# Performance work log

Hardware: AMD Instinct MI355X
Metric: run time of the kernel (lower is better)

## Reference

```python
import jax, jax.numpy as jnp
import numpy as np

VOL = 100.0  # cubic volume (100,100,100)


def _forward(x, positions, input_weights, features, output_weights,
             connection_radii, thresholds, n_iterations):
    # clamp positions into the volume (per-axis, min 0.1, max VOL-0.1)
    pos = jnp.clip(positions, 0.1, VOL - 0.1)                      # [N,3]
    radii = jnp.clip(connection_radii, 1.0, 50.0)                  # [N]
    # pairwise Euclidean distances via ||a||^2 + ||b||^2 - 2ab (avoids [N,N,3])
    sq = jnp.sum(pos * pos, axis=1)
    d2 = jnp.maximum(sq[:, None] + sq[None, :] - 2.0 * (pos @ pos.T), 0.0)
    pos_mask = d2 > 0.0
    dist = jnp.where(pos_mask, jnp.sqrt(jnp.where(pos_mask, d2, 1.0)), 0.0)  # [N,N]
    max_r = jnp.max(radii)
    conn_mask = (dist < max_r).astype(dist.dtype)
    atten = jnp.exp(-jnp.minimum(dist / (radii[:, None] + 1e-6), 20.0)) * conn_mask
    # feature similarity (F.normalize uses eps as a clamp-min on the norm)
    fn = features / jnp.maximum(jnp.linalg.norm(features, axis=1, keepdims=True), 1e-6)
    feat_sim = fn @ fn.T                                            # [N,N]
    cw = atten * (0.3 + 0.7 * jnp.clip(feat_sim, -1.0, 1.0))
    cw = cw / (jnp.sum(cw, axis=1, keepdims=True) + 1e-6)           # row-normalized [N,N]
    # spatial input / output gating along x-axis
    xc = jnp.clip(pos[:, 0] / VOL, 0.0, 1.0)                        # [N]
    iw = jnp.exp(-3.0 * xc)
    iw = iw / (jnp.sum(iw) + 1e-6)
    act = (x @ input_weights.T) * iw                                # [B,N]
    for _ in range(n_iterations):
        act = jnp.minimum(jax.nn.relu(act + act @ cw.T - thresholds), 100.0)
    ow = jnp.exp(3.0 * (xc - 1.0))
    ow = ow / (jnp.sum(ow) + 1e-6)
    return (act * ow) @ output_weights                              # [B,out]


def setup_inputs() -> dict:
    key = jax.random.key(0)
    ks = jax.random.split(key, 5)
    N, IN, OUT, FD, B = 8000, 784, 10, 32, 64
    return {
        "x": jax.random.normal(ks[0], (B, IN), jnp.float32),
        "positions": jax.random.uniform(ks[1], (N, 3), jnp.float32) * VOL,
        "input_weights": jax.random.normal(ks[2], (N, IN), jnp.float32) * 0.01,
        "features": jax.random.normal(ks[3], (N, FD), jnp.float32) * 0.1,
        "output_weights": jax.random.normal(ks[4], (N, OUT), jnp.float32) * 0.01,
        "connection_radii": jnp.ones((N,), jnp.float32) * 15.0,
        "thresholds": jnp.zeros((N,), jnp.float32),
        "n_iterations": 2,
    }


def reference(x, positions, input_weights, features, output_weights,
              connection_radii, thresholds, n_iterations):
    return _forward(x, positions, input_weights, features, output_weights,
                    connection_radii, thresholds, n_iterations)
```

## Files before the change

### kernel.cpp

```cpp
#include <hip/hip_runtime.h>
#include <hip/hip_bf16.h>
#include <math.h>

#define VOLF 100.0f
#define FD 32
#define OUT_DIM 10
#define MAXN 320
#define MAX_LAUNCH_ITERS 4
#define KSPLIT 7
#define ITILE 8
#define OB 128

__global__ __launch_bounds__(256) void k_pre(
    const float* __restrict__ positions, const float* __restrict__ radii_in,
    const float* __restrict__ features, float* __restrict__ posx4,
    float* __restrict__ radii, float* __restrict__ e_iw, float* __restrict__ e_ow,
    float* __restrict__ fn, float* __restrict__ scal, int N)
{
    int i = blockIdx.x * blockDim.x + threadIdx.x;
    float my_iw = 0.0f, my_ow = 0.0f, my_r = 0.0f;
    if (i < N) {
        float px = fminf(fmaxf(positions[3*i+0], 0.1f), VOLF - 0.1f);
        float py = fminf(fmaxf(positions[3*i+1], 0.1f), VOLF - 0.1f);
        float pz = fminf(fmaxf(positions[3*i+2], 0.1f), VOLF - 0.1f);
        float sq = px*px + py*py + pz*pz;
        posx4[4*i+0] = px; posx4[4*i+1] = py; posx4[4*i+2] = pz; posx4[4*i+3] = sq;
        float r = fminf(fmaxf(radii_in[i], 1.0f), 50.0f);
        radii[i] = r; my_r = r;
        float xc = fminf(fmaxf(px / VOLF, 0.0f), 1.0f);
        my_iw = expf(-3.0f * xc);
        my_ow = expf(3.0f * (xc - 1.0f));
        e_iw[i] = my_iw; e_ow[i] = my_ow;
        float s = 0.0f;
        #pragma unroll
        for (int k = 0; k < FD; k++) { float v = features[(size_t)i*FD + k]; s += v*v; }
        float nrm = fmaxf(sqrtf(s), 1e-6f);
        #pragma unroll
        for (int k = 0; k < FD; k++) fn[(size_t)i*FD + k] = features[(size_t)i*FD + k] / nrm;
    }
    __shared__ float red[256];
    red[threadIdx.x] = my_iw; __syncthreads();
    for (int s = 128; s > 0; s >>= 1) { if (threadIdx.x < s) red[threadIdx.x] += red[threadIdx.x + s]; __syncthreads(); }
    if (threadIdx.x == 0) atomicAdd(&scal[0], red[0]);
    __syncthreads();
    red[threadIdx.x] = my_ow; __syncthreads();
    for (int s = 128; s > 0; s >>= 1) { if (threadIdx.x < s) red[threadIdx.x] += red[threadIdx.x + s]; __syncthreads(); }
    if (threadIdx.x == 0) atomicAdd(&scal[1], red[0]);
    if (i < N) atomicMax((int*)&scal[2], __float_as_int(my_r));
}

__global__ __launch_bounds__(256) void k_xt(const float* __restrict__ x, float* __restrict__ xT,
                                            int B, int IN)
{
    int idx = blockIdx.x * blockDim.x + threadIdx.x;
    if (idx < B * IN) {
        int b = idx / IN, k = idx % IN;
        xT[(size_t)k * B + b] = x[idx];
    }
}

__global__ __launch_bounds__(256) void k_act0(
    const float* __restrict__ xT, const float* __restrict__ Wi,
    float* __restrict__ partial, int N, int IN)
{
    int wave = threadIdx.x >> 6, lane = threadIdx.x & 63;
    int i0 = blockIdx.x * 32 + wave * 8;
    int kchunk = IN / KSPLIT;
    int k0 = blockIdx.y * kchunk;
    int k1 = k0 + kchunk;
    float acc[8] = {0,0,0,0,0,0,0,0};
    for (int k = k0; k < k1; k += 4) {
        float xv0 = xT[(size_t)(k+0) * 64 + lane];
        float xv1 = xT[(size_t)(k+1) * 64 + lane];
        float xv2 = xT[(size_t)(k+2) * 64 + lane];
        float xv3 = xT[(size_t)(k+3) * 64 + lane];
        #pragma unroll
        for (int n = 0; n < 8; n++) {
            const float4 w = *(const float4*)(Wi + (size_t)(i0 + n) * IN + k);
            acc[n] += w.x * xv0 + w.y * xv1 + w.z * xv2 + w.w * xv3;
        }
    }
    #pragma unroll
    for (int n = 0; n < 8; n++)
        partial[((size_t)blockIdx.y * N + (i0 + n)) * 64 + lane] = acc[n];
}

__global__ __launch_bounds__(256) void k_act0_red(
    const float* __restrict__ partial, const float* __restrict__ e_iw,
    const float* __restrict__ scal, float* __restrict__ actA, int N)
{
    int idx = blockIdx.x * 256 + threadIdx.x;
    int i = idx >> 6;
    size_t stride = (size_t)N * 64;
    float s = 0.0f;
    #pragma unroll
    for (int ks = 0; ks < KSPLIT; ks++) s += partial[ks * stride + idx];
    float inv = 1.0f / (scal[0] + 1e-6f);
    actA[idx] = s * (e_iw[i] * inv);
}

__global__ __launch_bounds__(256) void k_scan(
    const float* __restrict__ posx4, const float* __restrict__ scal,
    int* __restrict__ nbr_idx, float* __restrict__ nbr_w ,
    int* __restrict__ nbr_cnt, int N)
{
    int i0 = blockIdx.x * ITILE;
    __shared__ int cnt[ITILE];
    if (threadIdx.x < ITILE) cnt[threadIdx.x] = 0;
    __syncthreads();
    float4 pi[ITILE];
    #pragma unroll
    for (int t = 0; t < ITILE; t++) pi[t] = ((const float4*)posx4)[i0 + t];
    float maxr = __int_as_float(((const int*)scal)[2]);
    for (int j = threadIdx.x; j < N; j += 256) {
        float4 pj = ((const float4*)posx4)[j];
        #pragma unroll
        for (int t = 0; t < ITILE; t++) {
            float d2 = fmaxf(pi[t].w + pj.w - 2.0f*(pi[t].x*pj.x + pi[t].y*pj.y + pi[t].z*pj.z), 0.0f);
            float dist = (d2 > 0.0f) ? sqrtf(d2) : 0.0f;
            if (dist < maxr) {
                int pos = atomicAdd(&cnt[t], 1);
                if (pos < MAXN) {
                    nbr_idx[(size_t)(i0+t) * MAXN + pos] = j;
                    nbr_w [(size_t)(i0+t) * MAXN + pos] = dist;
                }
            }
        }
    }
    __syncthreads();
    if (threadIdx.x < ITILE) nbr_cnt[i0 + threadIdx.x] = min(cnt[threadIdx.x], MAXN);
}

__global__ __launch_bounds__(128) void k_weight(
    const float* __restrict__ fn, const float* __restrict__ radii,
    const int* __restrict__ nbr_idx, float* __restrict__ nbr_w ,
    const int* __restrict__ nbr_cnt, float* __restrict__ rowinv, int N)
{
    int i = blockIdx.x;
    __shared__ float4 fni[FD/4];
    __shared__ float red[128];
    if (threadIdx.x < FD/4) fni[threadIdx.x] = ((const float4*)(fn + (size_t)i * FD))[threadIdx.x];
    __syncthreads();
    float inv_ri = 1.0f / (radii[i] + 1e-6f);
    int cnt = nbr_cnt[i];
    float s = 0.0f;
    for (int e = threadIdx.x; e < cnt; e += 128) {
        int j     = nbr_idx[(size_t)i * MAXN + e];
        float dist= nbr_w [(size_t)i * MAXN + e];
        const float4* fnj = (const float4*)(fn + (size_t)j * FD);
        float fs = 0.0f;
        #pragma unroll
        for (int k = 0; k < FD/4; k++) {
            float4 a = fni[k], b = fnj[k];
            fs += a.x*b.x + a.y*b.y + a.z*b.z + a.w*b.w;
        }
        fs = fminf(fmaxf(fs, -1.0f), 1.0f);
        float w = expf(-fminf(dist * inv_ri, 20.0f)) * (0.3f + 0.7f * fs);
        nbr_w[(size_t)i * MAXN + e] = w;
        s += w;
    }
    red[threadIdx.x] = s; __syncthreads();
    for (int st = 64; st > 0; st >>= 1) { if (threadIdx.x < st) red[threadIdx.x] += red[threadIdx.x + st]; __syncthreads(); }
    if (threadIdx.x == 0) rowinv[i] = 1.0f / (red[0] + 1e-6f);
}

__global__ __launch_bounds__(256) void k_iter(
    const float* __restrict__ actIn, float* __restrict__ actOut,
    const int* __restrict__ nbr_idx, const float* __restrict__ nbr_w,
    const int* __restrict__ nbr_cnt, const float* __restrict__ rowinv,
    const float* __restrict__ thr,
    const int* __restrict__ nIterPtr, int iterIdx, int N)
{
    if (iterIdx >= min(*nIterPtr, MAX_LAUNCH_ITERS)) return;
    int i = blockIdx.x;
    int wave = threadIdx.x >> 6, lane = threadIdx.x & 63;
    int cnt = nbr_cnt[i];
    float acc = 0.0f;
    for (int e = wave; e < cnt; e += 4) {
        int j   = nbr_idx[(size_t)i * MAXN + e];
        float w = nbr_w [(size_t)i * MAXN + e];
        acc += actIn[(size_t)j * 64 + lane] * w;
    }
    __shared__ float redA[4 * 64];
    redA[wave * 64 + lane] = acc;
    __syncthreads();
    if (wave == 0) {
        float tot = redA[lane] + redA[64 + lane] + redA[128 + lane] + redA[192 + lane];
        float v = actIn[(size_t)i * 64 + lane] + tot * rowinv[i] - thr[i];
        v = fminf(fmaxf(v, 0.0f), 100.0f);
        actOut[(size_t)i * 64 + lane] = v;
    }
}

__global__ __launch_bounds__(256) void k_out1(
    const float* __restrict__ actA, const float* __restrict__ actB,
    const int* __restrict__ nIterPtr, const float* __restrict__ e_ow,
    const float* __restrict__ scal, const float* __restrict__ outW,
    float* __restrict__ outPart, int N)
{
    int m = min(*nIterPtr, MAX_LAUNCH_ITERS);
    const float* actF = (m & 1) ? actB : actA;
    int wave = threadIdx.x >> 6, lane = threadIdx.x & 63;
    float inv = 1.0f / (scal[1] + 1e-6f);
    float acc[OUT_DIM];
    #pragma unroll
    for (int o = 0; o < OUT_DIM; o++) acc[o] = 0.0f;
    for (int i = blockIdx.x * 4 + wave; i < N; i += OB * 4) {
        float a = actF[(size_t)i * 64 + lane] * (e_ow[i] * inv);
        const float* wo = outW + (size_t)i * OUT_DIM;
        #pragma unroll
        for (int o = 0; o < OUT_DIM; o++) acc[o] += a * wo[o];
    }
    __shared__ float red[4][OUT_DIM][64];
    #pragma unroll
    for (int o = 0; o < OUT_DIM; o++) red[wave][o][lane] = acc[o];
    __syncthreads();
    if (wave == 0) {
        #pragma unroll
        for (int o = 0; o < OUT_DIM; o++) {
            float s = red[0][o][lane] + red[1][o][lane] + red[2][o][lane] + red[3][o][lane];
            outPart[((size_t)blockIdx.x * OUT_DIM + o) * 64 + lane] = s;
        }
    }
}

__global__ __launch_bounds__(256) void k_out2(
    const float* __restrict__ outPart, float* __restrict__ out)
{
    int t = blockIdx.x * 256 + threadIdx.x;
    if (t >= 64 * OUT_DIM) return;
    int b = t / OUT_DIM, o = t % OUT_DIM;
    float s = 0.0f;
    for (int blk = 0; blk < OB; blk++)
        s += outPart[((size_t)blk * OUT_DIM + o) * 64 + b];
    out[t] = s;
}

extern "C" void kernel_launch(void* const* d_in, const int* in_sizes, int n_in,
                              void* d_out, int out_size, void* d_ws, size_t ws_size,
                              hipStream_t stream)
{
    const float* x        = (const float*)d_in[0];
    const float* positions= (const float*)d_in[1];
    const float* Win      = (const float*)d_in[2];
    const float* features = (const float*)d_in[3];
    const float* Wout     = (const float*)d_in[4];
    const float* radii_in = (const float*)d_in[5];
    const float* thr      = (const float*)d_in[6];
    const int*   nIter    = (const int*)  d_in[7];

    const int N  = in_sizes[5];
    const int IN = in_sizes[2] / N;
    const int B  = in_sizes[0] / IN;
    (void)B;

    float* ws = (float*)d_ws;
    size_t off = 0;
    auto alloc = [&](size_t nfloats) { size_t cur = off; off += (nfloats + 63) & ~(size_t)63; return cur; };
    float* xT      = ws + alloc((size_t)B * IN);
    float* posx4   = ws + alloc((size_t)N * 4);
    float* radii   = ws + alloc(N);
    float* e_iw    = ws + alloc(N);
    float* e_ow    = ws + alloc(N);
    float* rowinv  = ws + alloc(N);
    float* scal    = ws + alloc(4);
    float* outPart = ws + alloc((size_t)OB * OUT_DIM * 64);
    float* fn      = ws + alloc((size_t)N * FD);
    float* actA    = ws + alloc((size_t)N * 64);
    float* actB    = ws + alloc((size_t)N * 64);
    float* nbr_w   = ws + alloc((size_t)N * MAXN);
    int*   nbr_idx = (int*)(ws + alloc((size_t)N * MAXN));
    int*   nbr_cnt = (int*)(ws + alloc(N));
    float* partial = nbr_w;

    hipMemsetAsync(scal, 0, 4 * sizeof(float), stream);

    k_pre<<<(N + 255) / 256, 256, 0, stream>>>(positions, radii_in, features,
                                               posx4, radii, e_iw, e_ow, fn, scal, N);
    k_xt<<<(B * IN + 255) / 256, 256, 0, stream>>>(x, xT, B, IN);
    k_act0<<<dim3(N / 32, KSPLIT), 256, 0, stream>>>(xT, Win, partial, N, IN);
    k_act0_red<<<(N * 64) / 256, 256, 0, stream>>>(partial, e_iw, scal, actA, N);
    k_scan<<<N / ITILE, 256, 0, stream>>>(posx4, scal, nbr_idx, nbr_w, nbr_cnt, N);
    k_weight<<<N, 128, 0, stream>>>(fn, radii, nbr_idx, nbr_w, nbr_cnt, rowinv, N);

    float* bufs[2] = {actA, actB};
    for (int it = 0; it < MAX_LAUNCH_ITERS; it++) {
        k_iter<<<N, 256, 0, stream>>>(bufs[it & 1], bufs[(it + 1) & 1],
                                      nbr_idx, nbr_w, nbr_cnt, rowinv, thr, nIter, it, N);
    }
    k_out1<<<OB, 256, 0, stream>>>(actA, actB, nIter, e_ow, scal, Wout, outPart, N);
    k_out2<<<3, 256, 0, stream>>>(outPart, (float*)d_out);
}
```

Before: 296.2 us.

## Stage input-weight and x tiles in shared memory for act0 GEMM

The input projection kernel now loads a 64-row by 112-column tile of the input weights and the matching 112-column slice of transposed x into LDS. Each wave then computes 16 output rows per lane from shared memory instead of doing strided global float4 loads per row. This cuts redundant global traffic and raises per-thread work, at the cost of about 57KB of LDS per block, which limits occupancy. The K chunk size of 112 is hardcoded and assumes IN=784 split into seven chunks.

```diff
diff --git a/kernel.cpp b/kernel.cpp
--- a/kernel.cpp
+++ b/kernel.cpp
@@ -8,6 +8,8 @@
 #define MAXN 320
 #define MAX_LAUNCH_ITERS 4
 #define KSPLIT 7
+#define BM 64
+#define BKQ 28
 #define ITILE 8
 #define OB 128
 
@@ -63,26 +65,46 @@
     const float* __restrict__ xT, const float* __restrict__ Wi,
     float* __restrict__ partial, int N, int IN)
 {
-    int wave = threadIdx.x >> 6, lane = threadIdx.x & 63;
-    int i0 = blockIdx.x * 32 + wave * 8;
-    int kchunk = IN / KSPLIT;
-    int k0 = blockIdx.y * kchunk;
-    int k1 = k0 + kchunk;
-    float acc[8] = {0,0,0,0,0,0,0,0};
-    for (int k = k0; k < k1; k += 4) {
-        float xv0 = xT[(size_t)(k+0) * 64 + lane];
-        float xv1 = xT[(size_t)(k+1) * 64 + lane];
-        float xv2 = xT[(size_t)(k+2) * 64 + lane];
-        float xv3 = xT[(size_t)(k+3) * 64 + lane];
-        #pragma unroll
-        for (int n = 0; n < 8; n++) {
-            const float4 w = *(const float4*)(Wi + (size_t)(i0 + n) * IN + k);
-            acc[n] += w.x * xv0 + w.y * xv1 + w.z * xv2 + w.w * xv3;
-        }
-    }
-    #pragma unroll
-    for (int n = 0; n < 8; n++)
-        partial[((size_t)blockIdx.y * N + (i0 + n)) * 64 + lane] = acc[n];
+    __shared__ float4 xs4[BKQ * 64];
+    __shared__ float  wt[BM * 112];
+    int t = threadIdx.x;
+    int i0 = blockIdx.x * BM;
+    int k0 = blockIdx.y * 112;
+    #pragma unroll
+    for (int fi = t; fi < BM * 28; fi += 256) {
+        int row = fi / 28, cq = fi % 28;
+        ((float4*)wt)[row * 28 + cq] = *(const float4*)(Wi + (size_t)(i0 + row) * IN + k0 + cq * 4);
+    }
+    {
+        int l = t & 63, q = t >> 6;
+        #pragma unroll
+        for (int kq = q; kq < BKQ; kq += 4) {
+            float4 v;
+            v.x = xT[(size_t)(k0 + 4*kq + 0) * 64 + l];
+            v.y = xT[(size_t)(k0 + 4*kq + 1) * 64 + l];
+            v.z = xT[(size_t)(k0 + 4*kq + 2) * 64 + l];
+            v.w = xT[(size_t)(k0 + 4*kq + 3) * 64 + l];
+            xs4[kq * 64 + l] = v;
+        }
+    }
+    __syncthreads();
+    int wave = t >> 6, lane = t & 63;
+    int nbase = wave * 16;
+    float acc[16];
+    #pragma unroll
+    for (int n = 0; n < 16; n++) acc[n] = 0.0f;
+    for (int kq = 0; kq < BKQ; kq++) {
+        float4 xv = xs4[kq * 64 + lane];
+        #pragma unroll
+        for (int n = 0; n < 16; n++) {
+            float4 w = ((const float4*)(wt + (nbase + n) * 112))[kq];
+            acc[n] += w.x * xv.x + w.y * xv.y + w.z * xv.z + w.w * xv.w;
+        }
+    }
+    size_t base = ((size_t)blockIdx.y * N + (i0 + nbase)) * 64 + lane;
+    #pragma unroll
+    for (int n = 0; n < 16; n++)
+        partial[base + (size_t)n * 64] = acc[n];
 }
 
 __global__ __launch_bounds__(256) void k_act0_red(
@@ -278,7 +300,7 @@
     k_pre<<<(N + 255) / 256, 256, 0, stream>>>(positions, radii_in, features,
                                                posx4, radii, e_iw, e_ow, fn, scal, N);
     k_xt<<<(B * IN + 255) / 256, 256, 0, stream>>>(x, xT, B, IN);
-    k_act0<<<dim3(N / 32, KSPLIT), 256, 0, stream>>>(xT, Win, partial, N, IN);
+    k_act0<<<dim3(N / BM, KSPLIT), 256, 0, stream>>>(xT, Win, partial, N, IN);
     k_act0_red<<<(N * 64) / 256, 256, 0, stream>>>(partial, e_iw, scal, actA, N);
     k_scan<<<N / ITILE, 256, 0, stream>>>(posx4, scal, nbr_idx, nbr_w, nbr_cnt, N);
     k_weight<<<N, 128, 0, stream>>>(fn, radii, nbr_idx, nbr_w, nbr_cnt, rowinv, N);
```

After: 250.5 us. 15.4% less time.
